# Kernel tuning notes

Measured on AMD Instinct MI355X. Metric: run time of the kernel, lower is better.

The kernel has to match this reference:

```python
import jax, jax.numpy as jnp
import numpy as np

N_ATOMS = 1000
BOX_L = 30.0      # cubic cell edge (Angstrom)
MAX_CUTOFF = 8.0  # max(cutoff)


def _np_cart(a, b, c):
    # numpy equivalent of torch.cartesian_prod for 3 1-D arrays
    g = np.meshgrid(a, b, c, indexing='ij')
    return np.stack(g, axis=-1).reshape(-1, 3)


def _np_get_shifts(cell, cutoff):
    # mirrors TorchNeighborListRangeSeparated._get_shifts (pbc=True on all axes)
    recip = np.linalg.inv(cell).T
    inv_len = np.linalg.norm(recip, axis=1)
    nrep = np.ceil(cutoff * inv_len).astype(np.int64)
    r1 = np.arange(1, nrep[0] + 1, dtype=np.float64)
    r2 = np.arange(1, nrep[1] + 1, dtype=np.float64)
    r3 = np.arange(1, nrep[2] + 1, dtype=np.float64)
    o = np.zeros(1, dtype=np.float64)
    return np.concatenate([
        _np_cart(r1, r2, r3), _np_cart(r1, r2, o), _np_cart(r1, r2, -r3),
        _np_cart(r1, o, r3), _np_cart(r1, o, o), _np_cart(r1, o, -r3),
        _np_cart(r1, -r2, r3), _np_cart(r1, -r2, o), _np_cart(r1, -r2, -r3),
        _np_cart(o, r2, r3), _np_cart(o, r2, o), _np_cart(o, r2, -r3),
        _np_cart(o, o, r3)], axis=0)


def setup_inputs() -> dict:
    key = jax.random.key(0)
    cell_np = np.eye(3) * BOX_L
    shifts = jnp.asarray(_np_get_shifts(cell_np, MAX_CUTOFF), dtype=jnp.float32)  # [13,3]
    positions = jax.random.uniform(key, (N_ATOMS, 3), dtype=jnp.float32) * BOX_L
    return {
        "positions": positions,
        "cell": jnp.asarray(cell_np, dtype=jnp.float32),
        "shifts": shifts,
        "cutoffs": jnp.array([4.0, 8.0], dtype=jnp.float32),
    }


def reference(positions, cell, shifts, cutoffs):
    """PBC-aware pairwise distance^2 + per-cutoff neighbor masks.

    Returns:
      d2:    [P] squared distances over all candidate pairs
             (N*(N-1)/2 in-cell pairs followed by S*N*N shifted-image pairs)
      masks: [n_cutoffs, P] int32 in-cutoff indicator (d2 < cutoff^2)
    """
    n = positions.shape[0]
    # in-cell pairs (torch.combinations -> i<j)
    iu, ju = jnp.triu_indices(n, k=1)
    rij_c = positions[iu] - positions[ju]                       # [Pc,3]
    d2_c = jnp.sum(rij_c * rij_c, axis=-1)                      # [Pc]
    # shifted-image pairs: all (shift, i, j)
    shift_values = shifts @ cell                                # [S,3]
    rij_o = (positions[None, :, None, :] - positions[None, None, :, :]
             + shift_values[:, None, None, :])                  # [S,N,N,3]
    d2_o = jnp.sum(rij_o * rij_o, axis=-1).reshape(-1)          # [S*N*N]
    d2 = jnp.concatenate([d2_c, d2_o], axis=0)                  # [P]
    masks = (d2[None, :] < (cutoffs ** 2)[:, None]).astype(jnp.int32)
    return d2, masks
```

## Files before the change

### kernel.cpp

```cpp
#include <hip/hip_runtime.h>
#include <math.h>


__global__ void __launch_bounds__(256) nbr_kernel(
    const float* __restrict__ pos,
    const float* __restrict__ cell,
    const float* __restrict__ shifts,
    const float* __restrict__ cutoffs,
    int ncut, int n,
    float* __restrict__ out, long long P, long long Pc)
{
    long long p0 = ((long long)blockIdx.x * 256 + threadIdx.x) << 2;
    if (p0 >= P) return;

    double cut2[4];
    for (int c = 0; c < ncut; ++c) { double cv = (double)cutoffs[c]; cut2[c] = cv * cv; }

    float d2f[4];
    float mf[4][4];

    if (p0 >= Pc) {
        long long q = p0 - Pc;
        unsigned nn = (unsigned)n * (unsigned)n;
        unsigned s  = (unsigned)((unsigned long long)q / nn);
        unsigned r  = (unsigned)((unsigned long long)q - (unsigned long long)s * nn);
        unsigned i  = r / (unsigned)n;
        unsigned j0 = r - i * (unsigned)n;

        double s0 = (double)shifts[3*s+0], s1 = (double)shifts[3*s+1], s2 = (double)shifts[3*s+2];
        double sv0 = s0 * (double)cell[0] + s1 * (double)cell[3] + s2 * (double)cell[6];
        double sv1 = s0 * (double)cell[1] + s1 * (double)cell[4] + s2 * (double)cell[7];
        double sv2 = s0 * (double)cell[2] + s1 * (double)cell[5] + s2 * (double)cell[8];

        double pix = (double)pos[3*i+0];
        double piy = (double)pos[3*i+1];
        double piz = (double)pos[3*i+2];

        const float4* pj = (const float4*)(pos + 3 * j0);
        float4 a = pj[0], b = pj[1], c4 = pj[2];
        float jx[4] = {a.x, a.w, b.z, c4.y};
        float jy[4] = {a.y, b.x, b.w, c4.z};
        float jz[4] = {a.z, b.y, c4.x, c4.w};

        for (int k = 0; k < 4; ++k) {
            double dx = (pix - (double)jx[k]) + sv0;
            double dy = (piy - (double)jy[k]) + sv1;
            double dz = (piz - (double)jz[k]) + sv2;
            double d2 = dx*dx + dy*dy + dz*dz;
            d2f[k] = (float)d2;
            for (int c = 0; c < ncut; ++c) mf[c][k] = (d2 < cut2[c]) ? 1.0f : 0.0f;
        }
    } else {
        long long tn = 2LL * n - 1;
        for (int k = 0; k < 4; ++k) {
            long long p = p0 + k;
            double D = (double)(tn * tn) - 8.0 * (double)p;
            long long i = (long long)(((double)tn - sqrt(D)) * 0.5);
            if (i < 0) i = 0;
            if (i > n - 2) i = n - 2;
            while ((i + 1) * (tn - (i + 1)) / 2 <= p) ++i;
            while (i * (tn - i) / 2 > p) --i;
            long long j = p - i * (tn - i) / 2 + i + 1;

            double dx = (double)pos[3*i+0] - (double)pos[3*j+0];
            double dy = (double)pos[3*i+1] - (double)pos[3*j+1];
            double dz = (double)pos[3*i+2] - (double)pos[3*j+2];
            double d2 = dx*dx + dy*dy + dz*dz;
            d2f[k] = (float)d2;
            for (int c = 0; c < ncut; ++c) mf[c][k] = (d2 < cut2[c]) ? 1.0f : 0.0f;
        }
    }

    *(float4*)(out + p0) = make_float4(d2f[0], d2f[1], d2f[2], d2f[3]);
    for (int c = 0; c < ncut; ++c)
        *(float4*)(out + (long long)(c + 1) * P + p0) =
            make_float4(mf[c][0], mf[c][1], mf[c][2], mf[c][3]);
}

__global__ void __launch_bounds__(256) nbr_kernel_scalar(
    const float* __restrict__ pos,
    const float* __restrict__ cell,
    const float* __restrict__ shifts,
    const float* __restrict__ cutoffs,
    int ncut, int n,
    float* __restrict__ out, long long P, long long Pc)
{
    long long p = (long long)blockIdx.x * 256 + threadIdx.x;
    if (p >= P) return;

    double cut2[4];
    for (int c = 0; c < ncut; ++c) { double cv = (double)cutoffs[c]; cut2[c] = cv * cv; }

    double d2;
    if (p >= Pc) {
        long long q = p - Pc;
        unsigned long long nn = (unsigned long long)n * n;
        unsigned s = (unsigned)(q / nn);
        unsigned long long r = q - (unsigned long long)s * nn;
        unsigned i = (unsigned)(r / n);
        unsigned j = (unsigned)(r - (unsigned long long)i * n);
        double s0 = (double)shifts[3*s+0], s1 = (double)shifts[3*s+1], s2 = (double)shifts[3*s+2];
        double sv0 = s0*(double)cell[0] + s1*(double)cell[3] + s2*(double)cell[6];
        double sv1 = s0*(double)cell[1] + s1*(double)cell[4] + s2*(double)cell[7];
        double sv2 = s0*(double)cell[2] + s1*(double)cell[5] + s2*(double)cell[8];
        double dx = ((double)pos[3*i+0] - (double)pos[3*j+0]) + sv0;
        double dy = ((double)pos[3*i+1] - (double)pos[3*j+1]) + sv1;
        double dz = ((double)pos[3*i+2] - (double)pos[3*j+2]) + sv2;
        d2 = dx*dx + dy*dy + dz*dz;
    } else {
        long long tn = 2LL * n - 1;
        double D = (double)(tn * tn) - 8.0 * (double)p;
        long long i = (long long)(((double)tn - sqrt(D)) * 0.5);
        if (i < 0) i = 0;
        if (i > n - 2) i = n - 2;
        while ((i + 1) * (tn - (i + 1)) / 2 <= p) ++i;
        while (i * (tn - i) / 2 > p) --i;
        long long j = p - i * (tn - i) / 2 + i + 1;
        double dx = (double)pos[3*i+0] - (double)pos[3*j+0];
        double dy = (double)pos[3*i+1] - (double)pos[3*j+1];
        double dz = (double)pos[3*i+2] - (double)pos[3*j+2];
        d2 = dx*dx + dy*dy + dz*dz;
    }
    out[p] = (float)d2;
    for (int c = 0; c < ncut; ++c)
        out[(long long)(c + 1) * P + p] = (d2 < cut2[c]) ? 1.0f : 0.0f;
}

extern "C" void kernel_launch(void* const* d_in, const int* in_sizes, int n_in,
                              void* d_out, int out_size, void* d_ws, size_t ws_size,
                              hipStream_t stream)
{
    const float* pos     = (const float*)d_in[0];
    const float* cell    = (const float*)d_in[1];
    const float* shifts  = (const float*)d_in[2];
    const float* cutoffs = (const float*)d_in[3];
    int n    = in_sizes[0] / 3;
    int S    = in_sizes[2] / 3;
    int ncut = in_sizes[3];

    long long Pc = (long long)n * (n - 1) / 2;
    long long P  = Pc + (long long)S * n * n;
    float* out = (float*)d_out;

    if ((n & 3) == 0) {
        long long chunks = P >> 2;
        int blocks = (int)((chunks + 255) / 256);
        nbr_kernel<<<blocks, 256, 0, stream>>>(pos, cell, shifts, cutoffs,
                                               ncut, n, out, P, Pc);
    } else {
        int blocks = (int)((P + 255) / 256);
        nbr_kernel_scalar<<<blocks, 256, 0, stream>>>(pos, cell, shifts, cutoffs,
                                                      ncut, n, out, P, Pc);
    }
}
```

Before: 169.2 us.

## Map shifted-image pairs onto a 2D grid and use nontemporal stores

Replaces the flat 1D launch with a 2D grid. blockIdx.y selects the shift, blockIdx.x selects atom i, and each thread handles four consecutive j values, with one extra y-row covering the in-cell triangular pairs. This removes the per-thread 64-bit division and modulo used to decode (s, i, j) from a linear index. All output writes become nontemporal vector stores to reduce cache pollution from the large write-only stream. In exchange, some threads and blocks in the launch do no work: threads past j=n are wasted, and the triangular row launches as many x-blocks as there are atoms.

Measured after the change: 183.1 us. +8.2%, slower.

```diff
diff --git a/kernel.cpp b/kernel.cpp
--- a/kernel.cpp
+++ b/kernel.cpp
@@ -2,30 +2,36 @@
 #include <math.h>
 
 
-__global__ void __launch_bounds__(256) nbr_kernel(
+typedef float f32x4 __attribute__((ext_vector_type(4)));
+
+__device__ __forceinline__ void nt_store4(float* p, float a, float b, float c, float d)
+{
+    f32x4 v = {a, b, c, d};
+    __builtin_nontemporal_store(v, (f32x4*)p);
+}
+
+__global__ void __launch_bounds__(256) nbr_kernel_grid(
     const float* __restrict__ pos,
     const float* __restrict__ cell,
     const float* __restrict__ shifts,
     const float* __restrict__ cutoffs,
-    int ncut, int n,
+    int ncut, int n, int S,
     float* __restrict__ out, long long P, long long Pc)
 {
-    long long p0 = ((long long)blockIdx.x * 256 + threadIdx.x) << 2;
-    if (p0 >= P) return;
-
     double cut2[4];
-    for (int c = 0; c < ncut; ++c) { double cv = (double)cutoffs[c]; cut2[c] = cv * cv; }
+#pragma unroll
+    for (int c = 0; c < 4; ++c)
+        if (c < ncut) { double cv = (double)cutoffs[c]; cut2[c] = cv * cv; }
 
     float d2f[4];
     float mf[4][4];
 
-    if (p0 >= Pc) {
-        long long q = p0 - Pc;
-        unsigned nn = (unsigned)n * (unsigned)n;
-        unsigned s  = (unsigned)((unsigned long long)q / nn);
-        unsigned r  = (unsigned)((unsigned long long)q - (unsigned long long)s * nn);
-        unsigned i  = r / (unsigned)n;
-        unsigned j0 = r - i * (unsigned)n;
+    if ((int)blockIdx.y < S) {
+        int s = (int)blockIdx.y;
+        int i = (int)blockIdx.x;
+        if (i >= n) return;
+        int j0 = (int)threadIdx.x << 2;
+        if (j0 >= n) return;
 
         double s0 = (double)shifts[3*s+0], s1 = (double)shifts[3*s+1], s2 = (double)shifts[3*s+2];
         double sv0 = s0 * (double)cell[0] + s1 * (double)cell[3] + s2 * (double)cell[6];
@@ -42,16 +48,33 @@
         float jy[4] = {a.y, b.x, b.w, c4.z};
         float jz[4] = {a.z, b.y, c4.x, c4.w};
 
+#pragma unroll
         for (int k = 0; k < 4; ++k) {
             double dx = (pix - (double)jx[k]) + sv0;
             double dy = (piy - (double)jy[k]) + sv1;
             double dz = (piz - (double)jz[k]) + sv2;
             double d2 = dx*dx + dy*dy + dz*dz;
             d2f[k] = (float)d2;
-            for (int c = 0; c < ncut; ++c) mf[c][k] = (d2 < cut2[c]) ? 1.0f : 0.0f;
+#pragma unroll
+            for (int c = 0; c < 4; ++c)
+                if (c < ncut) mf[c][k] = (d2 < cut2[c]) ? 1.0f : 0.0f;
         }
+
+        long long base = Pc + ((long long)s * (long long)n + (long long)i) * (long long)n
+                         + (long long)j0;
+        nt_store4(out + base, d2f[0], d2f[1], d2f[2], d2f[3]);
+#pragma unroll
+        for (int c = 0; c < 4; ++c)
+            if (c < ncut)
+                nt_store4(out + (long long)(c + 1) * P + base,
+                          mf[c][0], mf[c][1], mf[c][2], mf[c][3]);
     } else {
+        long long chunk = (long long)blockIdx.x * 256 + threadIdx.x;
+        long long p0 = chunk << 2;
+        if (p0 >= Pc) return;
+
         long long tn = 2LL * n - 1;
+#pragma unroll
         for (int k = 0; k < 4; ++k) {
             long long p = p0 + k;
             double D = (double)(tn * tn) - 8.0 * (double)p;
@@ -67,14 +90,18 @@
             double dz = (double)pos[3*i+2] - (double)pos[3*j+2];
             double d2 = dx*dx + dy*dy + dz*dz;
             d2f[k] = (float)d2;
-            for (int c = 0; c < ncut; ++c) mf[c][k] = (d2 < cut2[c]) ? 1.0f : 0.0f;
+#pragma unroll
+            for (int c = 0; c < 4; ++c)
+                if (c < ncut) mf[c][k] = (d2 < cut2[c]) ? 1.0f : 0.0f;
         }
+
+        nt_store4(out + p0, d2f[0], d2f[1], d2f[2], d2f[3]);
+#pragma unroll
+        for (int c = 0; c < 4; ++c)
+            if (c < ncut)
+                nt_store4(out + (long long)(c + 1) * P + p0,
+                          mf[c][0], mf[c][1], mf[c][2], mf[c][3]);
     }
-
-    *(float4*)(out + p0) = make_float4(d2f[0], d2f[1], d2f[2], d2f[3]);
-    for (int c = 0; c < ncut; ++c)
-        *(float4*)(out + (long long)(c + 1) * P + p0) =
-            make_float4(mf[c][0], mf[c][1], mf[c][2], mf[c][3]);
 }
 
 __global__ void __launch_bounds__(256) nbr_kernel_scalar(
@@ -143,10 +170,12 @@
     float* out = (float*)d_out;
 
     if ((n & 3) == 0) {
-        long long chunks = P >> 2;
-        int blocks = (int)((chunks + 255) / 256);
-        nbr_kernel<<<blocks, 256, 0, stream>>>(pos, cell, shifts, cutoffs,
-                                               ncut, n, out, P, Pc);
+        long long triuChunks = Pc >> 2;
+        int triuBlocks = (int)((triuChunks + 255) / 256);
+        int gx = (n > triuBlocks) ? n : triuBlocks;
+        dim3 grid((unsigned)gx, (unsigned)(S + 1));
+        nbr_kernel_grid<<<grid, 256, 0, stream>>>(pos, cell, shifts, cutoffs,
+                                                  ncut, n, S, out, P, Pc);
     } else {
         int blocks = (int)((P + 255) / 256);
         nbr_kernel_scalar<<<blocks, 256, 0, stream>>>(pos, cell, shifts, cutoffs,
```
